# Performance work log

Hardware: AMD Instinct MI355X
Metric: run time of the kernel (lower is better)

## Reference

```python
import jax, jax.numpy as jnp
import numpy as np

MAG = 1.0
TAU = 0.5
B, D, C = 8192, 256, 128


def setup_inputs() -> dict:
    key = jax.random.key(0)
    k1, k2 = jax.random.split(key)
    outputs = jax.random.normal(k1, (B, D), dtype=jnp.float32)
    labels = jax.random.normal(k2, (B, C), dtype=jnp.float32)
    return {"outputs": outputs, "labels": labels}


def reference(outputs, labels):
    # Cosine-similarity matrix of labels, min-max normalized to [0, 1]
    norm2labels = labels / (jnp.linalg.norm(labels, axis=1, keepdims=True) + 1e-12)
    sim_mat = norm2labels @ norm2labels.T  # [B, B]
    sim_mat = (sim_mat - sim_mat.min()) / (sim_mat.max() - sim_mat.min())

    # Pairwise Euclidean distances of outputs via the Gram trick
    # ||x_i - x_j||^2 = ||x_i||^2 + ||x_j||^2 - 2 <x_i, x_j>
    sq = jnp.sum(outputs * outputs, axis=1)  # [B]
    d2 = sq[:, None] + sq[None, :] - 2.0 * (outputs @ outputs.T)  # [B, B]
    d2 = jnp.maximum(d2, 0.0)
    nz = d2 > 0.0
    # safe sqrt: zero (diagonal) entries get distance 0 with zero gradient,
    # matching torch.norm's subgradient at 0
    eud = jnp.sqrt(jnp.where(nz, d2, 1.0)) * nz
    eud = eud / eud.max()

    distance = eud + sim_mat  # [B, B]
    pos_mask = sim_mat > TAU

    # Per-row masked log-sum-exp terms (distance in [0, 2], no overflow risk)
    pos_loss = jnp.log(jnp.sum(jnp.where(pos_mask, jnp.exp(distance), 0.0), axis=1))
    neg_loss = jnp.log(jnp.sum(jnp.where(pos_mask, 0.0, jnp.exp(MAG - distance)), axis=1))

    # clamp negatives (and -inf from empty masks) to 0, as the original `if < 0` does
    loss = jnp.maximum(pos_loss, 0.0) + jnp.maximum(neg_loss, 0.0)
    return jnp.mean(loss)
```

## Files before the change

### kernel.cpp

```cpp
#include <hip/hip_runtime.h>
#include <hip/hip_bf16.h>


#define B_N 8192
#define NT   64
#define TILE 128
#define NTRI 2080
#define WS_NEEDED 142704704ull

typedef __attribute__((ext_vector_type(8))) short bf16x8;
typedef __attribute__((ext_vector_type(4))) float f32x4;
typedef __attribute__((ext_vector_type(2))) _Float16 f16x2;
typedef __attribute__((ext_vector_type(4))) unsigned u32x4;

typedef const __attribute__((address_space(1))) void g_void;
typedef __attribute__((address_space(3))) void l_void;

__device__ __forceinline__ unsigned fenc(float f) {
    unsigned u = __float_as_uint(f);
    return (u & 0x80000000u) ? ~u : (u | 0x80000000u);
}
__device__ __forceinline__ float fdec(unsigned k) {
    unsigned u = (k & 0x80000000u) ? (k ^ 0x80000000u) : ~k;
    return __uint_as_float(u);
}
__device__ __forceinline__ unsigned pack2(float a, float b) {
    f16x2 p; p[0] = (_Float16)a; p[1] = (_Float16)b;
    return *(unsigned*)&p;
}

__device__ __forceinline__ void tile_decode(int b, int& bi, int& bj) {
    int si, sj, ti, tj;
    if (b < 544) {
        int sb = b / 136, w = b - sb * 136;
        int i = 0;
        while (w >= 16 - i) { w -= 16 - i; i++; }
        si = sb; sj = sb; ti = i; tj = i + w;
    } else {
        int q = (b - 544) >> 8, w = (b - 544) & 255;
        int i = 0;
        while (q >= 3 - i) { q -= 3 - i; i++; }
        si = i; sj = i + 1 + q;
        ti = w >> 4; tj = w & 15;
    }
    bi = si * 16 + ti; bj = sj * 16 + tj;
}

__global__ __launch_bounds__(256) void prep_kernel(
    const float* __restrict__ outputs, const float* __restrict__ labels,
    __hip_bfloat16* __restrict__ Obp, __hip_bfloat16* __restrict__ Lnp,
    float* __restrict__ sq, float* __restrict__ pos_sums,
    float* __restrict__ neg_sums, unsigned* __restrict__ stats) {
    int g = blockIdx.x, tid = threadIdx.x;
    int rl = tid >> 4, c = tid & 15;
    int row = g * 16 + rl;
    __shared__ __align__(16) short tO[16][264];
    __shared__ __align__(16) short tL[16][136];

    float s = 0.f;
    #pragma unroll
    for (int k = 0; k < 4; k++) {
        f32x4 v = *(const f32x4*)&outputs[(size_t)row * 256 + c * 16 + k * 4];
        s += v[0]*v[0] + v[1]*v[1] + v[2]*v[2] + v[3]*v[3];
        __hip_bfloat16 b4[4];
        #pragma unroll
        for (int i = 0; i < 4; i++) b4[i] = __float2bfloat16(v[i]);
        *(uint2*)&tO[rl][c * 16 + k * 4] = *(uint2*)b4;
    }
    #pragma unroll
    for (int m = 1; m < 16; m <<= 1) s += __shfl_xor(s, m);
    if (c == 0) sq[row] = s;

    float ls = 0.f;
    f32x4 u0 = *(const f32x4*)&labels[(size_t)row * 128 + c * 8];
    f32x4 u1 = *(const f32x4*)&labels[(size_t)row * 128 + c * 8 + 4];
    ls += u0[0]*u0[0] + u0[1]*u0[1] + u0[2]*u0[2] + u0[3]*u0[3];
    ls += u1[0]*u1[0] + u1[1]*u1[1] + u1[2]*u1[2] + u1[3]*u1[3];
    #pragma unroll
    for (int m = 1; m < 16; m <<= 1) ls += __shfl_xor(ls, m);
    float inv = 1.f / (sqrtf(ls) + 1e-12f);
    {
        __hip_bfloat16 b4[4];
        #pragma unroll
        for (int i = 0; i < 4; i++) b4[i] = __float2bfloat16(u0[i] * inv);
        *(uint2*)&tL[rl][c * 8] = *(uint2*)b4;
        #pragma unroll
        for (int i = 0; i < 4; i++) b4[i] = __float2bfloat16(u1[i] * inv);
        *(uint2*)&tL[rl][c * 8 + 4] = *(uint2*)b4;
    }
    if (tid < 16) { pos_sums[g * 16 + tid] = 0.f; neg_sums[g * 16 + tid] = 0.f; }
    if (g == 0 && tid == 0) {
        stats[0] = 0xFFFFFFFFu; stats[1] = 0u; stats[2] = 0u;
    }
    __syncthreads();

    #pragma unroll
    for (int q = 0; q < 2; q++) {
        int sl = tid * 2 + q;
        int o = sl >> 4, rr = sl & 15;
        uint4 d = *(uint4*)&tO[rr][o * 8];
        *(uint4*)&Obp[(size_t)g * 4096 + (size_t)sl * 8] = d;
    }
    {
        int o = tid >> 4, rr = tid & 15;
        uint4 d = *(uint4*)&tL[rr][o * 8];
        *(uint4*)&Lnp[(size_t)g * 2048 + (size_t)tid * 8] = d;
    }
}

template<int KD8>
__device__ __forceinline__ void stage_slice(
    const short* __restrict__ P, int g0, int o0, short* L, int tid) {
    #pragma unroll
    for (int p = 0; p < 4; p++) {
        int u = p * 256 + tid;
        int gl = u >> 7, off = u & 127;
        size_t gu = ((size_t)(g0 + gl) * KD8 + o0) * 16 + off;
        __builtin_amdgcn_global_load_lds((g_void*)(P + gu * 8),
                                         (l_void*)(L + (size_t)u * 8), 16, 0, 0);
    }
}

__device__ __forceinline__ void mfma_slice(
    const short* As, const short* Bs, int wm4, int wn4,
    int l15, int quad, f32x4 (&acc)[4][4]) {
    #pragma unroll
    for (int kc = 0; kc < 2; kc++) {
        bf16x8 a[4], b[4];
        #pragma unroll
        for (int mi = 0; mi < 4; mi++)
            a[mi] = *(const bf16x8*)&As[((wm4 + mi) * 128
                                         + (kc * 4 + quad) * 16 + l15) * 8];
        #pragma unroll
        for (int ni = 0; ni < 4; ni++)
            b[ni] = *(const bf16x8*)&Bs[((wn4 + ni) * 128
                                         + (kc * 4 + quad) * 16 + l15) * 8];
        #pragma unroll
        for (int mi = 0; mi < 4; mi++)
            #pragma unroll
            for (int ni = 0; ni < 4; ni++)
                acc[mi][ni] = __builtin_amdgcn_mfma_f32_16x16x32_bf16(
                    a[mi], b[ni], acc[mi][ni], 0, 0, 0);
    }
}

__device__ __forceinline__ void zero_acc(f32x4 (&acc)[4][4]) {
    #pragma unroll
    for (int mi = 0; mi < 4; mi++)
        #pragma unroll
        for (int ni = 0; ni < 4; ni++) {
            f32x4 z = {0.f, 0.f, 0.f, 0.f};
            acc[mi][ni] = z;
        }
}

template<int KD8, int NS>
__device__ __forceinline__ void gram_staged(
    const short* __restrict__ P, int gA0, int gB0,
    short* As, short* Bs, int tid, int wm4, int wn4,
    int l15, int quad, f32x4 (&acc)[4][4]) {
    #pragma unroll
    for (int s = 0; s < NS; s++) {
        __syncthreads();
        stage_slice<KD8>(P, gA0, s * 8, As, tid);
        stage_slice<KD8>(P, gB0, s * 8, Bs, tid);
        __syncthreads();
        mfma_slice(As, Bs, wm4, wn4, l15, quad, acc);
    }
}

__global__ __launch_bounds__(256, 2) void stats_kernel(
    const short* __restrict__ Lnp, const short* __restrict__ Obp,
    const float* __restrict__ sq, unsigned* __restrict__ stats,
    unsigned* __restrict__ simT, unsigned* __restrict__ eudT, int store) {
    int bi, bj;
    tile_decode(blockIdx.x, bi, bj);
    int tid = threadIdx.x, lane = tid & 63, wid = tid >> 6;
    int wm = (wid >> 1) * 64, wn = (wid & 1) * 64;
    int wm4 = (wid >> 1) * 4, wn4 = (wid & 1) * 4;
    int l15 = lane & 15, quad = lane >> 4;
    int rB = bi * TILE, cB = bj * TILE;
    size_t tB = (size_t)blockIdx.x * 8192 + (size_t)tid * 4;

    __shared__ __align__(16) short As[1024 * 8];
    __shared__ __align__(16) short Bs[1024 * 8];

    float lmin = 1e30f, lmax = -1e30f, dmax = 0.f;
    f32x4 acc[4][4];

    zero_acc(acc);
    gram_staged<16, 2>(Lnp, bi * 8, bj * 8, As, Bs, tid, wm4, wn4, l15, quad, acc);
    #pragma unroll
    for (int mi = 0; mi < 4; mi++) {
        u32x4 v0, v1;
        #pragma unroll
        for (int ni = 0; ni < 4; ni++)
            #pragma unroll
            for (int h = 0; h < 2; h++) {
                float s0 = acc[mi][ni][2 * h], s1 = acc[mi][ni][2 * h + 1];
                lmin = fminf(lmin, fminf(s0, s1));
                lmax = fmaxf(lmax, fmaxf(s0, s1));
                int j = ni * 2 + h;
                unsigned pk = pack2(s0, s1);
                if (j < 4) v0[j] = pk; else v1[j - 4] = pk;
            }
        if (store) {
            __builtin_nontemporal_store(v0, (u32x4*)(simT + tB + (mi * 2 + 0) * 1024));
            __builtin_nontemporal_store(v1, (u32x4*)(simT + tB + (mi * 2 + 1) * 1024));
        }
    }

    zero_acc(acc);
    gram_staged<32, 4>(Obp, bi * 8, bj * 8, As, Bs, tid, wm4, wn4, l15, quad, acc);
    float sqj[4];
    #pragma unroll
    for (int ni = 0; ni < 4; ni++) sqj[ni] = sq[cB + wn + ni * 16 + l15];
    #pragma unroll
    for (int mi = 0; mi < 4; mi++) {
        f32x4 sqi = *(const f32x4*)&sq[rB + wm + mi * 16 + quad * 4];
        u32x4 v0, v1;
        #pragma unroll
        for (int ni = 0; ni < 4; ni++)
            #pragma unroll
            for (int h = 0; h < 2; h++) {
                float d20 = fmaxf(sqi[2*h]   + sqj[ni] - 2.f * acc[mi][ni][2*h],   0.f);
                float d21 = fmaxf(sqi[2*h+1] + sqj[ni] - 2.f * acc[mi][ni][2*h+1], 0.f);
                dmax = fmaxf(dmax, fmaxf(d20, d21));
                float e0 = (d20 > 0.f) ? sqrtf(d20) : 0.f;
                float e1 = (d21 > 0.f) ? sqrtf(d21) : 0.f;
                int j = ni * 2 + h;
                unsigned pk = pack2(e0, e1);
                if (j < 4) v0[j] = pk; else v1[j - 4] = pk;
            }
        if (store) {
            __builtin_nontemporal_store(v0, (u32x4*)(eudT + tB + (mi * 2 + 0) * 1024));
            __builtin_nontemporal_store(v1, (u32x4*)(eudT + tB + (mi * 2 + 1) * 1024));
        }
    }

    #pragma unroll
    for (int m = 1; m < 64; m <<= 1) {
        lmin = fminf(lmin, __shfl_xor(lmin, m));
        lmax = fmaxf(lmax, __shfl_xor(lmax, m));
        dmax = fmaxf(dmax, __shfl_xor(dmax, m));
    }
    __shared__ float red[3][4];
    if ((tid & 63) == 0) { red[0][wid] = lmin; red[1][wid] = lmax; red[2][wid] = dmax; }
    __syncthreads();
    if (tid == 0) {
        lmin = fminf(fminf(red[0][0], red[0][1]), fminf(red[0][2], red[0][3]));
        lmax = fmaxf(fmaxf(red[1][0], red[1][1]), fmaxf(red[1][2], red[1][3]));
        dmax = fmaxf(fmaxf(red[2][0], red[2][1]), fmaxf(red[2][2], red[2][3]));
        atomicMin(&stats[0], fenc(lmin));
        atomicMax(&stats[1], fenc(lmax));
        atomicMax(&stats[2], fenc(dmax));
    }
}

__global__ __launch_bounds__(256) void loss_stream_kernel(
    const unsigned* __restrict__ simT, const unsigned* __restrict__ eudT,
    const unsigned* __restrict__ stats,
    float* __restrict__ pos_sums, float* __restrict__ neg_sums) {
    int bi, bj;
    tile_decode(blockIdx.x, bi, bj);
    int tid = threadIdx.x, lane = tid & 63, wid = tid >> 6;
    int wm = (wid >> 1) * 64, wn = (wid & 1) * 64;
    int l15 = lane & 15, quad = lane >> 4;
    size_t tB = (size_t)blockIdx.x * 8192 + (size_t)tid * 4;

    float smin = fdec(stats[0]);
    float smax = fdec(stats[1]);
    float d2max = fdec(stats[2]);
    float invr = 1.f / (smax - smin);
    float invem = rsqrtf(d2max);

    __shared__ float rP[TILE][2], rN[TILE][2];
    __shared__ float cP[TILE][2], cN[TILE][2];
    float cpsum[4] = {0.f, 0.f, 0.f, 0.f};
    float cnsum[4] = {0.f, 0.f, 0.f, 0.f};

    #pragma unroll
    for (int mi = 0; mi < 4; mi++) {
        u32x4 s0 = __builtin_nontemporal_load((const u32x4*)(simT + tB + (mi * 2 + 0) * 1024));
        u32x4 s1 = __builtin_nontemporal_load((const u32x4*)(simT + tB + (mi * 2 + 1) * 1024));
        u32x4 e0 = __builtin_nontemporal_load((const u32x4*)(eudT + tB + (mi * 2 + 0) * 1024));
        u32x4 e1 = __builtin_nontemporal_load((const u32x4*)(eudT + tB + (mi * 2 + 1) * 1024));
        float ps[4] = {0.f, 0.f, 0.f, 0.f};
        float ns[4] = {0.f, 0.f, 0.f, 0.f};
        #pragma unroll
        for (int j = 0; j < 8; j++) {
            unsigned sv = (j < 4) ? s0[j] : s1[j - 4];
            unsigned ev = (j < 4) ? e0[j] : e1[j - 4];
            int ni = j >> 1, h = j & 1;
            f16x2 spair = *(f16x2*)&sv;
            f16x2 epair = *(f16x2*)&ev;
            #pragma unroll
            for (int e = 0; e < 2; e++) {
                float sn = ((float)spair[e] - smin) * invr;
                float dist = (float)epair[e] * invem + sn;
                bool pos = sn > 0.5f;
                float pv = pos ? __expf(dist) : 0.f;
                float nv = pos ? 0.f : __expf(1.0f - dist);
                ps[2 * h + e] += pv;  ns[2 * h + e] += nv;
                cpsum[ni] += pv;  cnsum[ni] += nv;
            }
        }
        #pragma unroll
        for (int r = 0; r < 4; r++) {
            #pragma unroll
            for (int m = 1; m < 16; m <<= 1) {
                ps[r] += __shfl_xor(ps[r], m);
                ns[r] += __shfl_xor(ns[r], m);
            }
            if (l15 == 0) {
                int rr = wm + mi * 16 + quad * 4 + r;
                rP[rr][wid & 1] = ps[r];
                rN[rr][wid & 1] = ns[r];
            }
        }
    }
    #pragma unroll
    for (int ni = 0; ni < 4; ni++) {
        #pragma unroll
        for (int m = 16; m < 64; m <<= 1) {
            cpsum[ni] += __shfl_xor(cpsum[ni], m);
            cnsum[ni] += __shfl_xor(cnsum[ni], m);
        }
        if (quad == 0) {
            int cc = wn + ni * 16 + l15;
            cP[cc][wid >> 1] = cpsum[ni];
            cN[cc][wid >> 1] = cnsum[ni];
        }
    }
    __syncthreads();
    if (tid < TILE) {
        atomicAdd(&pos_sums[bi * TILE + tid], rP[tid][0] + rP[tid][1]);
        atomicAdd(&neg_sums[bi * TILE + tid], rN[tid][0] + rN[tid][1]);
        if (bi != bj) {
            atomicAdd(&pos_sums[bj * TILE + tid], cP[tid][0] + cP[tid][1]);
            atomicAdd(&neg_sums[bj * TILE + tid], cN[tid][0] + cN[tid][1]);
        }
    }
}

__global__ __launch_bounds__(256, 2) void loss_recompute_kernel(
    const short* __restrict__ Lnp, const short* __restrict__ Obp,
    const float* __restrict__ sq, const unsigned* __restrict__ stats,
    float* __restrict__ pos_sums, float* __restrict__ neg_sums) {
    int bi, bj;
    tile_decode(blockIdx.x, bi, bj);
    int tid = threadIdx.x, lane = tid & 63, wid = tid >> 6;
    int wm = (wid >> 1) * 64, wn = (wid & 1) * 64;
    int wm4 = (wid >> 1) * 4, wn4 = (wid & 1) * 4;
    int l15 = lane & 15, quad = lane >> 4;
    int rB = bi * TILE, cB = bj * TILE;

    __shared__ __align__(16) short As[1024 * 8];
    __shared__ __align__(16) short Bs[1024 * 8];
    __shared__ unsigned simW[256 * 33];
    __shared__ float rP[TILE][2], rN[TILE][2];
    __shared__ float cP[TILE][2], cN[TILE][2];
    unsigned* my = &simW[tid * 33];

    f32x4 acc[4][4];

    zero_acc(acc);
    gram_staged<16, 2>(Lnp, bi * 8, bj * 8, As, Bs, tid, wm4, wn4, l15, quad, acc);
    #pragma unroll
    for (int mi = 0; mi < 4; mi++)
        #pragma unroll
        for (int ni = 0; ni < 4; ni++) {
            my[(mi * 4 + ni) * 2 + 0] = pack2(acc[mi][ni][0], acc[mi][ni][1]);
            my[(mi * 4 + ni) * 2 + 1] = pack2(acc[mi][ni][2], acc[mi][ni][3]);
        }

    zero_acc(acc);
    gram_staged<32, 4>(Obp, bi * 8, bj * 8, As, Bs, tid, wm4, wn4, l15, quad, acc);

    float smin = fdec(stats[0]);
    float smax = fdec(stats[1]);
    float d2max = fdec(stats[2]);
    float invr = 1.f / (smax - smin);
    float invem = rsqrtf(d2max);

    float sqj[4];
    #pragma unroll
    for (int ni = 0; ni < 4; ni++) sqj[ni] = sq[cB + wn + ni * 16 + l15];
    float cpsum[4] = {0.f, 0.f, 0.f, 0.f};
    float cnsum[4] = {0.f, 0.f, 0.f, 0.f};

    #pragma unroll
    for (int mi = 0; mi < 4; mi++) {
        f32x4 sqi = *(const f32x4*)&sq[rB + wm + mi * 16 + quad * 4];
        float ps[4] = {0.f, 0.f, 0.f, 0.f};
        float ns[4] = {0.f, 0.f, 0.f, 0.f};
        #pragma unroll
        for (int ni = 0; ni < 4; ni++) {
            f16x2 s01 = ((const f16x2*)my)[(mi * 4 + ni) * 2 + 0];
            f16x2 s23 = ((const f16x2*)my)[(mi * 4 + ni) * 2 + 1];
            #pragma unroll
            for (int r = 0; r < 4; r++) {
                float sraw = (r < 2) ? (float)s01[r] : (float)s23[r - 2];
                float sn = (sraw - smin) * invr;
                float g = acc[mi][ni][r];
                float d2 = fmaxf(sqi[r] + sqj[ni] - 2.f * g, 0.f);
                float eud = (d2 > 0.f) ? sqrtf(d2) * invem : 0.f;
                float dist = eud + sn;
                bool pos = sn > 0.5f;
                float pv = pos ? __expf(dist) : 0.f;
                float nv = pos ? 0.f : __expf(1.0f - dist);
                ps[r] += pv;  ns[r] += nv;
                cpsum[ni] += pv;  cnsum[ni] += nv;
            }
        }
        #pragma unroll
        for (int r = 0; r < 4; r++) {
            #pragma unroll
            for (int m = 1; m < 16; m <<= 1) {
                ps[r] += __shfl_xor(ps[r], m);
                ns[r] += __shfl_xor(ns[r], m);
            }
            if (l15 == 0) {
                int rr = wm + mi * 16 + quad * 4 + r;
                rP[rr][wid & 1] = ps[r];
                rN[rr][wid & 1] = ns[r];
            }
        }
    }
    #pragma unroll
    for (int ni = 0; ni < 4; ni++) {
        #pragma unroll
        for (int m = 16; m < 64; m <<= 1) {
            cpsum[ni] += __shfl_xor(cpsum[ni], m);
            cnsum[ni] += __shfl_xor(cnsum[ni], m);
        }
        if (quad == 0) {
            int cc = wn + ni * 16 + l15;
            cP[cc][wid >> 1] = cpsum[ni];
            cN[cc][wid >> 1] = cnsum[ni];
        }
    }
    __syncthreads();
    if (tid < TILE) {
        atomicAdd(&pos_sums[bi * TILE + tid], rP[tid][0] + rP[tid][1]);
        atomicAdd(&neg_sums[bi * TILE + tid], rN[tid][0] + rN[tid][1]);
        if (bi != bj) {
            atomicAdd(&pos_sums[bj * TILE + tid], cP[tid][0] + cP[tid][1]);
            atomicAdd(&neg_sums[bj * TILE + tid], cN[tid][0] + cN[tid][1]);
        }
    }
}

__global__ __launch_bounds__(256) void finalize_kernel(
    const float* __restrict__ pos_sums, const float* __restrict__ neg_sums,
    float* __restrict__ out) {
    int t = threadIdx.x;
    float acc = 0.f;
    for (int i = t; i < B_N; i += 256) {
        float p = pos_sums[i], n = neg_sums[i];
        float pl = fmaxf(logf(p), 0.f);
        float nl = (n > 0.f) ? fmaxf(logf(n), 0.f) : 0.f;
        acc += pl + nl;
    }
    #pragma unroll
    for (int m = 1; m < 64; m <<= 1) acc += __shfl_xor(acc, m);
    __shared__ float w4[4];
    if ((t & 63) == 0) w4[t >> 6] = acc;
    __syncthreads();
    if (t == 0) out[0] = (w4[0] + w4[1] + w4[2] + w4[3]) / (float)B_N;
}

extern "C" void kernel_launch(void* const* d_in, const int* in_sizes, int n_in,
                              void* d_out, int out_size, void* d_ws, size_t ws_size,
                              hipStream_t stream) {
    const float* outputs = (const float*)d_in[0];
    const float* labels  = (const float*)d_in[1];
    float* out = (float*)d_out;
    char* ws = (char*)d_ws;
    __hip_bfloat16* Obp = (__hip_bfloat16*)(ws);
    __hip_bfloat16* Lnp = (__hip_bfloat16*)(ws + 4194304);
    float* sq           = (float*)(ws + 6291456);
    float* pos_sums     = (float*)(ws + 6324224);
    float* neg_sums     = (float*)(ws + 6356992);
    unsigned* stats     = (unsigned*)(ws + 6389760);
    unsigned* simT      = (unsigned*)(ws + 6389824);
    unsigned* eudT      = (unsigned*)(ws + 74547264);
    int big = (ws_size >= WS_NEEDED) ? 1 : 0;

    prep_kernel<<<B_N / 16, 256, 0, stream>>>(outputs, labels, Obp, Lnp, sq,
                                              pos_sums, neg_sums, stats);
    stats_kernel<<<NTRI, 256, 0, stream>>>((const short*)Lnp, (const short*)Obp,
                                           sq, stats, simT, eudT, big);
    if (big)
        loss_stream_kernel<<<NTRI, 256, 0, stream>>>(simT, eudT, stats,
                                                     pos_sums, neg_sums);
    else
        loss_recompute_kernel<<<NTRI, 256, 0, stream>>>((const short*)Lnp,
                                                        (const short*)Obp,
                                                        sq, stats,
                                                        pos_sums, neg_sums);
    finalize_kernel<<<1, 256, 0, stream>>>(pos_sums, neg_sums, out);
}
```

Baseline: 209.6 us.

## Compute stats with 256x256 super-tiles and double-buffered LDS staging

The stats kernel now processes 256x256 super-tiles with 512 threads (8 waves, 128x64 per wave), launching 528 upper-triangular blocks instead of 2080 128x128 tiles. Each block stages K-slices into double-buffered LDS via global_load_lds and overlaps the next slice's loads with MFMA on the current one. Results are still written in the original 128-tile layout through a tile_encode mapping, and the redundant lower-triangle sub-tile on diagonal super-tiles is skipped. Larger tiles give more operand reuse and fewer blocks. In exchange, each wave holds many more accumulator registers and each block uses 128 KB of LDS, which limits occupancy, and the diagonal super-tiles compute one sub-tile that is thrown away.

```diff
diff --git a/kernel.cpp b/kernel.cpp
--- a/kernel.cpp
+++ b/kernel.cpp
@@ -3,9 +3,9 @@
 
 
 #define B_N 8192
-#define NT   64
 #define TILE 128
 #define NTRI 2080
+#define NSUP 528
 #define WS_NEEDED 142704704ull
 
 typedef __attribute__((ext_vector_type(8))) short bf16x8;
@@ -46,6 +46,13 @@
     bi = si * 16 + ti; bj = sj * 16 + tj;
 }
 
+__device__ __forceinline__ int tile_encode(int bi, int bj) {
+    int si = bi >> 4, sj = bj >> 4, ti = bi & 15, tj = bj & 15;
+    if (si == sj) return si * 136 + ti * 16 - (ti * (ti - 1)) / 2 + (tj - ti);
+    int off = 3 * si - (si * (si - 1)) / 2 + (sj - si - 1);
+    return 544 + off * 256 + ti * 16 + tj;
+}
+
 __global__ __launch_bounds__(256) void prep_kernel(
     const float* __restrict__ outputs, const float* __restrict__ labels,
     __hip_bfloat16* __restrict__ Obp, __hip_bfloat16* __restrict__ Lnp,
@@ -169,72 +176,167 @@
     }
 }
 
-__global__ __launch_bounds__(256, 2) void stats_kernel(
+__device__ __forceinline__ void stage512(const short* __restrict__ P, int g0,
+                                         int kd8, int o0, short* L, int tid) {
+    #pragma unroll
+    for (int p = 0; p < 4; p++) {
+        int u = p * 512 + tid;
+        int gl = u >> 7, off = u & 127;
+        size_t gu = ((size_t)(g0 + gl) * kd8 + o0) * 16 + off;
+        __builtin_amdgcn_global_load_lds((g_void*)(P + gu * 8),
+                                         (l_void*)(L + (size_t)u * 8), 16, 0, 0);
+    }
+}
+
+__device__ __forceinline__ void mfma64(const short* As, const short* Bs,
+                                       int wr8, int wc4, int l15, int quad,
+                                       f32x4 (&acc)[8][4]) {
+    #pragma unroll
+    for (int kc = 0; kc < 2; kc++) {
+        bf16x8 a[8], b[4];
+        #pragma unroll
+        for (int am = 0; am < 8; am++)
+            a[am] = *(const bf16x8*)&As[((wr8 + am) * 128
+                                         + (kc * 4 + quad) * 16 + l15) * 8];
+        #pragma unroll
+        for (int bn = 0; bn < 4; bn++)
+            b[bn] = *(const bf16x8*)&Bs[((wc4 + bn) * 128
+                                         + (kc * 4 + quad) * 16 + l15) * 8];
+        #pragma unroll
+        for (int am = 0; am < 8; am++)
+            #pragma unroll
+            for (int bn = 0; bn < 4; bn++)
+                acc[am][bn] = __builtin_amdgcn_mfma_f32_16x16x32_bf16(
+                    a[am], b[bn], acc[am][bn], 0, 0, 0);
+    }
+}
+
+__device__ __forceinline__ void zero_acc8(f32x4 (&acc)[8][4]) {
+    #pragma unroll
+    for (int mi = 0; mi < 8; mi++)
+        #pragma unroll
+        for (int ni = 0; ni < 4; ni++) {
+            f32x4 z = {0.f, 0.f, 0.f, 0.f};
+            acc[mi][ni] = z;
+        }
+}
+
+#define VMCNT(n) asm volatile("s_waitcnt vmcnt(" #n ")" ::: "memory")
+#define BAR() __builtin_amdgcn_s_barrier()
+
+__global__ __launch_bounds__(512, 2) void stats_kernel(
     const short* __restrict__ Lnp, const short* __restrict__ Obp,
     const float* __restrict__ sq, unsigned* __restrict__ stats,
     unsigned* __restrict__ simT, unsigned* __restrict__ eudT, int store) {
-    int bi, bj;
-    tile_decode(blockIdx.x, bi, bj);
+    int bt = blockIdx.x, BI = 0;
+    while (bt >= 32 - BI) { bt -= 32 - BI; BI++; }
+    int BJ = BI + bt;
+
     int tid = threadIdx.x, lane = tid & 63, wid = tid >> 6;
-    int wm = (wid >> 1) * 64, wn = (wid & 1) * 64;
-    int wm4 = (wid >> 1) * 4, wn4 = (wid & 1) * 4;
+    int wr = wid >> 2, wc = wid & 3;
     int l15 = lane & 15, quad = lane >> 4;
-    int rB = bi * TILE, cB = bj * TILE;
-    size_t tB = (size_t)blockIdx.x * 8192 + (size_t)tid * 4;
-
-    __shared__ __align__(16) short As[1024 * 8];
-    __shared__ __align__(16) short Bs[1024 * 8];
+    int wr8 = wr * 8, wc4 = wc * 4;
+    int wcH = wc >> 1, wcL = wc & 1;
+
+    __shared__ __align__(16) short As[2][16384];
+    __shared__ __align__(16) short Bs[2][16384];
+    __shared__ float red[3][8];
+
+    int gA = BI * 16, gB = BJ * 16;
+    bool dostore = store && !(BI == BJ && wr == 1 && wcH == 0);
+    int b128 = tile_encode(BI * 2 + wr, BJ * 2 + wcH);
+    size_t blkbase = (size_t)b128 * 8192;
 
     float lmin = 1e30f, lmax = -1e30f, dmax = 0.f;
-    f32x4 acc[4][4];
-
-    zero_acc(acc);
-    gram_staged<16, 2>(Lnp, bi * 8, bj * 8, As, Bs, tid, wm4, wn4, l15, quad, acc);
-    #pragma unroll
-    for (int mi = 0; mi < 4; mi++) {
-        u32x4 v0, v1;
-        #pragma unroll
-        for (int ni = 0; ni < 4; ni++)
-            #pragma unroll
-            for (int h = 0; h < 2; h++) {
-                float s0 = acc[mi][ni][2 * h], s1 = acc[mi][ni][2 * h + 1];
-                lmin = fminf(lmin, fminf(s0, s1));
-                lmax = fmaxf(lmax, fmaxf(s0, s1));
-                int j = ni * 2 + h;
-                unsigned pk = pack2(s0, s1);
-                if (j < 4) v0[j] = pk; else v1[j - 4] = pk;
-            }
-        if (store) {
-            __builtin_nontemporal_store(v0, (u32x4*)(simT + tB + (mi * 2 + 0) * 1024));
-            __builtin_nontemporal_store(v1, (u32x4*)(simT + tB + (mi * 2 + 1) * 1024));
-        }
-    }
-
-    zero_acc(acc);
-    gram_staged<32, 4>(Obp, bi * 8, bj * 8, As, Bs, tid, wm4, wn4, l15, quad, acc);
-    float sqj[4];
-    #pragma unroll
-    for (int ni = 0; ni < 4; ni++) sqj[ni] = sq[cB + wn + ni * 16 + l15];
-    #pragma unroll
-    for (int mi = 0; mi < 4; mi++) {
-        f32x4 sqi = *(const f32x4*)&sq[rB + wm + mi * 16 + quad * 4];
-        u32x4 v0, v1;
-        #pragma unroll
-        for (int ni = 0; ni < 4; ni++)
-            #pragma unroll
-            for (int h = 0; h < 2; h++) {
-                float d20 = fmaxf(sqi[2*h]   + sqj[ni] - 2.f * acc[mi][ni][2*h],   0.f);
-                float d21 = fmaxf(sqi[2*h+1] + sqj[ni] - 2.f * acc[mi][ni][2*h+1], 0.f);
-                dmax = fmaxf(dmax, fmaxf(d20, d21));
-                float e0 = (d20 > 0.f) ? sqrtf(d20) : 0.f;
-                float e1 = (d21 > 0.f) ? sqrtf(d21) : 0.f;
-                int j = ni * 2 + h;
-                unsigned pk = pack2(e0, e1);
-                if (j < 4) v0[j] = pk; else v1[j - 4] = pk;
-            }
-        if (store) {
-            __builtin_nontemporal_store(v0, (u32x4*)(eudT + tB + (mi * 2 + 0) * 1024));
-            __builtin_nontemporal_store(v1, (u32x4*)(eudT + tB + (mi * 2 + 1) * 1024));
+    f32x4 acc[8][4];
+
+    zero_acc8(acc);
+    stage512(Lnp, gA, 16, 0, &As[0][0], tid);
+    stage512(Lnp, gB, 16, 0, &Bs[0][0], tid);
+    stage512(Lnp, gA, 16, 8, &As[1][0], tid);
+    stage512(Lnp, gB, 16, 8, &Bs[1][0], tid);
+    VMCNT(8); BAR();
+    mfma64(&As[0][0], &Bs[0][0], wr8, wc4, l15, quad, acc);
+    VMCNT(0); BAR();
+    mfma64(&As[1][0], &Bs[1][0], wr8, wc4, l15, quad, acc);
+
+    #pragma unroll
+    for (int am = 0; am < 8; am++) {
+        int tid128 = (((am >> 2) << 1) | wcL) * 64 + lane;
+        #pragma unroll
+        for (int bh = 0; bh < 2; bh++) {
+            u32x4 v;
+            #pragma unroll
+            for (int b2 = 0; b2 < 2; b2++) {
+                int bn = bh * 2 + b2;
+                #pragma unroll
+                for (int h = 0; h < 2; h++) {
+                    float s0 = acc[am][bn][2 * h], s1 = acc[am][bn][2 * h + 1];
+                    lmin = fminf(lmin, fminf(s0, s1));
+                    lmax = fmaxf(lmax, fmaxf(s0, s1));
+                    v[b2 * 2 + h] = pack2(s0, s1);
+                }
+            }
+            if (dostore)
+                __builtin_nontemporal_store(v, (u32x4*)(simT + blkbase
+                    + ((am & 3) * 2 + bh) * 1024 + tid128 * 4));
+        }
+    }
+    BAR();
+
+    zero_acc8(acc);
+    stage512(Obp, gA, 32, 0, &As[0][0], tid);
+    stage512(Obp, gB, 32, 0, &Bs[0][0], tid);
+    stage512(Obp, gA, 32, 8, &As[1][0], tid);
+    stage512(Obp, gB, 32, 8, &Bs[1][0], tid);
+    VMCNT(8); BAR();
+    mfma64(&As[0][0], &Bs[0][0], wr8, wc4, l15, quad, acc);
+    VMCNT(0); BAR();
+    stage512(Obp, gA, 32, 16, &As[0][0], tid);
+    stage512(Obp, gB, 32, 16, &Bs[0][0], tid);
+    mfma64(&As[1][0], &Bs[1][0], wr8, wc4, l15, quad, acc);
+    VMCNT(0); BAR();
+    stage512(Obp, gA, 32, 24, &As[1][0], tid);
+    stage512(Obp, gB, 32, 24, &Bs[1][0], tid);
+    f32x4 sqi[8]; float sqj[4];
+    {
+        int rqa = BI * 256 + wr * 128 + quad * 4;
+        int cqa = BJ * 256 + wc * 64 + l15;
+        #pragma unroll
+        for (int am = 0; am < 8; am++)
+            sqi[am] = *(const f32x4*)&sq[rqa + am * 16];
+        #pragma unroll
+        for (int bn = 0; bn < 4; bn++)
+            sqj[bn] = sq[cqa + bn * 16];
+    }
+    mfma64(&As[0][0], &Bs[0][0], wr8, wc4, l15, quad, acc);
+    VMCNT(0); BAR();
+    mfma64(&As[1][0], &Bs[1][0], wr8, wc4, l15, quad, acc);
+
+    #pragma unroll
+    for (int am = 0; am < 8; am++) {
+        int tid128 = (((am >> 2) << 1) | wcL) * 64 + lane;
+        f32x4 si = sqi[am];
+        #pragma unroll
+        for (int bh = 0; bh < 2; bh++) {
+            u32x4 v;
+            #pragma unroll
+            for (int b2 = 0; b2 < 2; b2++) {
+                int bn = bh * 2 + b2;
+                float sj = sqj[bn];
+                #pragma unroll
+                for (int h = 0; h < 2; h++) {
+                    float d20 = fmaxf(si[2*h]   + sj - 2.f * acc[am][bn][2*h],   0.f);
+                    float d21 = fmaxf(si[2*h+1] + sj - 2.f * acc[am][bn][2*h+1], 0.f);
+                    dmax = fmaxf(dmax, fmaxf(d20, d21));
+                    float e0 = (d20 > 0.f) ? sqrtf(d20) : 0.f;
+                    float e1 = (d21 > 0.f) ? sqrtf(d21) : 0.f;
+                    v[b2 * 2 + h] = pack2(e0, e1);
+                }
+            }
+            if (dostore)
+                __builtin_nontemporal_store(v, (u32x4*)(eudT + blkbase
+                    + ((am & 3) * 2 + bh) * 1024 + tid128 * 4));
         }
     }
 
@@ -244,13 +346,16 @@
         lmax = fmaxf(lmax, __shfl_xor(lmax, m));
         dmax = fmaxf(dmax, __shfl_xor(dmax, m));
     }
-    __shared__ float red[3][4];
-    if ((tid & 63) == 0) { red[0][wid] = lmin; red[1][wid] = lmax; red[2][wid] = dmax; }
+    if (lane == 0) { red[0][wid] = lmin; red[1][wid] = lmax; red[2][wid] = dmax; }
     __syncthreads();
     if (tid == 0) {
-        lmin = fminf(fminf(red[0][0], red[0][1]), fminf(red[0][2], red[0][3]));
-        lmax = fmaxf(fmaxf(red[1][0], red[1][1]), fmaxf(red[1][2], red[1][3]));
-        dmax = fmaxf(fmaxf(red[2][0], red[2][1]), fmaxf(red[2][2], red[2][3]));
+        lmin = red[0][0]; lmax = red[1][0]; dmax = red[2][0];
+        #pragma unroll
+        for (int w = 1; w < 8; w++) {
+            lmin = fminf(lmin, red[0][w]);
+            lmax = fmaxf(lmax, red[1][w]);
+            dmax = fmaxf(dmax, red[2][w]);
+        }
         atomicMin(&stats[0], fenc(lmin));
         atomicMax(&stats[1], fenc(lmax));
         atomicMax(&stats[2], fenc(dmax));
@@ -489,7 +594,7 @@
 
     prep_kernel<<<B_N / 16, 256, 0, stream>>>(outputs, labels, Obp, Lnp, sq,
                                               pos_sums, neg_sums, stats);
-    stats_kernel<<<NTRI, 256, 0, stream>>>((const short*)Lnp, (const short*)Obp,
+    stats_kernel<<<NSUP, 512, 0, stream>>>((const short*)Lnp, (const short*)Obp,
                                            sq, stats, simT, eudT, big);
     if (big)
         loss_stream_kernel<<<NTRI, 256, 0, stream>>>(simT, eudT, stats,
```

After: 268.8 us. 28.2% more time.

## Double-buffer LDS staging in stats kernel and overlap loads with MFMA and epilogue

Applied to the files above, without the earlier changes.

Replaces the synchronous stage-then-compute loops in the stats kernel with a hand-scheduled double-buffered pipeline. Global-to-LDS slice loads for the next step, including the first output-Gram slices, are issued before the current MFMA slice and before the label epilogue, using explicit vmcnt waits and raw barriers. The aim is to hide global load latency behind MFMA and epilogue work. The cost is doubled LDS use (64KB per block), which may limit the two-blocks-per-CU occupancy, plus fragile hand-counted vmcnt values.

```diff
diff --git a/kernel.cpp b/kernel.cpp
--- a/kernel.cpp
+++ b/kernel.cpp
@@ -3,7 +3,6 @@
 
 
 #define B_N 8192
-#define NT   64
 #define TILE 128
 #define NTRI 2080
 #define WS_NEEDED 142704704ull
@@ -169,6 +168,10 @@
     }
 }
 
+#define VMCNT(n) asm volatile("s_waitcnt vmcnt(" #n ")" ::: "memory")
+#define BAR() __builtin_amdgcn_s_barrier()
+#define FENCE() asm volatile("" ::: "memory")
+
 __global__ __launch_bounds__(256, 2) void stats_kernel(
     const short* __restrict__ Lnp, const short* __restrict__ Obp,
     const float* __restrict__ sq, unsigned* __restrict__ stats,
@@ -182,14 +185,30 @@
     int rB = bi * TILE, cB = bj * TILE;
     size_t tB = (size_t)blockIdx.x * 8192 + (size_t)tid * 4;
 
-    __shared__ __align__(16) short As[1024 * 8];
-    __shared__ __align__(16) short Bs[1024 * 8];
+    __shared__ __align__(16) short As[2][8192];
+    __shared__ __align__(16) short Bs[2][8192];
+    __shared__ float red[3][4];
 
     float lmin = 1e30f, lmax = -1e30f, dmax = 0.f;
     f32x4 acc[4][4];
 
     zero_acc(acc);
-    gram_staged<16, 2>(Lnp, bi * 8, bj * 8, As, Bs, tid, wm4, wn4, l15, quad, acc);
+    stage_slice<16>(Lnp, bi * 8, 0, As[0], tid);
+    stage_slice<16>(Lnp, bj * 8, 0, Bs[0], tid);
+    stage_slice<16>(Lnp, bi * 8, 8, As[1], tid);
+    stage_slice<16>(Lnp, bj * 8, 8, Bs[1], tid);
+    VMCNT(8); BAR();
+    mfma_slice(As[0], Bs[0], wm4, wn4, l15, quad, acc);
+    BAR();
+    stage_slice<32>(Obp, bi * 8, 0, As[0], tid);
+    stage_slice<32>(Obp, bj * 8, 0, Bs[0], tid);
+    VMCNT(8); BAR();
+    mfma_slice(As[1], Bs[1], wm4, wn4, l15, quad, acc);
+    BAR();
+    stage_slice<32>(Obp, bi * 8, 8, As[1], tid);
+    stage_slice<32>(Obp, bj * 8, 8, Bs[1], tid);
+    FENCE();
+
     #pragma unroll
     for (int mi = 0; mi < 4; mi++) {
         u32x4 v0, v1;
@@ -211,13 +230,31 @@
     }
 
     zero_acc(acc);
-    gram_staged<32, 4>(Obp, bi * 8, bj * 8, As, Bs, tid, wm4, wn4, l15, quad, acc);
-    float sqj[4];
+    VMCNT(24); BAR();
+    mfma_slice(As[0], Bs[0], wm4, wn4, l15, quad, acc);
+    BAR();
+    stage_slice<32>(Obp, bi * 8, 16, As[0], tid);
+    stage_slice<32>(Obp, bj * 8, 16, Bs[0], tid);
+    FENCE();
+    float sqj[4]; f32x4 sqi4[4];
     #pragma unroll
     for (int ni = 0; ni < 4; ni++) sqj[ni] = sq[cB + wn + ni * 16 + l15];
     #pragma unroll
+    for (int mi = 0; mi < 4; mi++)
+        sqi4[mi] = *(const f32x4*)&sq[rB + wm + mi * 16 + quad * 4];
+    VMCNT(32); BAR();
+    mfma_slice(As[1], Bs[1], wm4, wn4, l15, quad, acc);
+    BAR();
+    stage_slice<32>(Obp, bi * 8, 24, As[1], tid);
+    stage_slice<32>(Obp, bj * 8, 24, Bs[1], tid);
+    VMCNT(8); BAR();
+    mfma_slice(As[0], Bs[0], wm4, wn4, l15, quad, acc);
+    VMCNT(0); BAR();
+    mfma_slice(As[1], Bs[1], wm4, wn4, l15, quad, acc);
+
+    #pragma unroll
     for (int mi = 0; mi < 4; mi++) {
-        f32x4 sqi = *(const f32x4*)&sq[rB + wm + mi * 16 + quad * 4];
+        f32x4 sqi = sqi4[mi];
         u32x4 v0, v1;
         #pragma unroll
         for (int ni = 0; ni < 4; ni++)
@@ -244,7 +281,6 @@
         lmax = fmaxf(lmax, __shfl_xor(lmax, m));
         dmax = fmaxf(dmax, __shfl_xor(dmax, m));
     }
-    __shared__ float red[3][4];
     if ((tid & 63) == 0) { red[0][wid] = lmin; red[1][wid] = lmax; red[2][wid] = dmax; }
     __syncthreads();
     if (tid == 0) {
```

Result: no change. 209.6 us (-0.0%).

## Rework stats kernel into 256x256 super-tiles with double-buffered async LDS staging

Applied to the files above, without the earlier changes.

The stats kernel now launches 528 blocks of 1024 threads, each covering a 256x256 upper-triangular super-tile made of four 128x128 sub-tiles, instead of 2080 blocks of 256 threads. Operand slices are loaded with global_load_lds into double-buffered shared memory under manual vmcnt waits, so the label and output Gram loads overlap MFMA work. Each staged A/B panel is reused across two sub-tiles. Stores are remapped through tile_encode so the existing loss kernel layout still holds, and the redundant lower sub-tile on diagonal blocks is skipped. The cost is a very large shared-memory footprint per block, lower occupancy, and fragile hand-counted vmcnt values.

```diff
diff --git a/kernel.cpp b/kernel.cpp
--- a/kernel.cpp
+++ b/kernel.cpp
@@ -3,9 +3,9 @@
 
 
 #define B_N 8192
-#define NT   64
 #define TILE 128
 #define NTRI 2080
+#define NSUP 528
 #define WS_NEEDED 142704704ull
 
 typedef __attribute__((ext_vector_type(8))) short bf16x8;
@@ -46,6 +46,13 @@
     bi = si * 16 + ti; bj = sj * 16 + tj;
 }
 
+__device__ __forceinline__ int tile_encode(int bi, int bj) {
+    int si = bi >> 4, sj = bj >> 4, ti = bi & 15, tj = bj & 15;
+    if (si == sj) return si * 136 + ti * 16 - (ti * (ti - 1)) / 2 + (tj - ti);
+    int off = 3 * si - (si * (si - 1)) / 2 + (sj - si - 1);
+    return 544 + off * 256 + ti * 16 + tj;
+}
+
 __global__ __launch_bounds__(256) void prep_kernel(
     const float* __restrict__ outputs, const float* __restrict__ labels,
     __hip_bfloat16* __restrict__ Obp, __hip_bfloat16* __restrict__ Lnp,
@@ -169,27 +176,67 @@
     }
 }
 
-__global__ __launch_bounds__(256, 2) void stats_kernel(
+__device__ __forceinline__ void stage1024(const short* __restrict__ P, int g0,
+                                          int kd8, int o0, short* L, int tid) {
+    #pragma unroll
+    for (int p = 0; p < 2; p++) {
+        int u = p * 1024 + tid;
+        int gl = u >> 7, off = u & 127;
+        size_t gu = ((size_t)(g0 + gl) * kd8 + o0) * 16 + off;
+        __builtin_amdgcn_global_load_lds((g_void*)(P + gu * 8),
+                                         (l_void*)(L + (size_t)u * 8), 16, 0, 0);
+    }
+}
+
+#define VMCNT(n) asm volatile("s_waitcnt vmcnt(" #n ")" ::: "memory")
+#define BAR() __builtin_amdgcn_s_barrier()
+#define FENCE() asm volatile("" ::: "memory")
+
+__global__ __launch_bounds__(1024, 4) void stats_kernel(
     const short* __restrict__ Lnp, const short* __restrict__ Obp,
     const float* __restrict__ sq, unsigned* __restrict__ stats,
     unsigned* __restrict__ simT, unsigned* __restrict__ eudT, int store) {
-    int bi, bj;
-    tile_decode(blockIdx.x, bi, bj);
+    int bt = blockIdx.x, BI = 0;
+    while (bt >= 32 - BI) { bt -= 32 - BI; BI++; }
+    int BJ = BI + bt;
+
     int tid = threadIdx.x, lane = tid & 63, wid = tid >> 6;
-    int wm = (wid >> 1) * 64, wn = (wid & 1) * 64;
-    int wm4 = (wid >> 1) * 4, wn4 = (wid & 1) * 4;
+    int wr = wid >> 2, wc = wid & 3;
+    int tr = wr >> 1, tc = wc >> 1;
     int l15 = lane & 15, quad = lane >> 4;
-    int rB = bi * TILE, cB = bj * TILE;
-    size_t tB = (size_t)blockIdx.x * 8192 + (size_t)tid * 4;
-
-    __shared__ __align__(16) short As[1024 * 8];
-    __shared__ __align__(16) short Bs[1024 * 8];
+    int wm4 = wr * 4, wn4 = wc * 4;
+
+    __shared__ __align__(16) short As[2][16384];
+    __shared__ __align__(16) short Bs[2][16384];
+    __shared__ float red[3][16];
+
+    int gA = BI * 16, gB = BJ * 16;
+    bool dostore = store && !(BI == BJ && tr == 1 && tc == 0);
+    int b128 = tile_encode(BI * 2 + tr, BJ * 2 + tc);
+    int wid0 = ((wr & 1) << 1) | (wc & 1);
+    int tid128 = wid0 * 64 + lane;
+    size_t blkbase = (size_t)b128 * 8192 + (size_t)tid128 * 4;
 
     float lmin = 1e30f, lmax = -1e30f, dmax = 0.f;
     f32x4 acc[4][4];
 
     zero_acc(acc);
-    gram_staged<16, 2>(Lnp, bi * 8, bj * 8, As, Bs, tid, wm4, wn4, l15, quad, acc);
+    stage1024(Lnp, gA, 16, 0, &As[0][0], tid);
+    stage1024(Lnp, gB, 16, 0, &Bs[0][0], tid);
+    stage1024(Lnp, gA, 16, 8, &As[1][0], tid);
+    stage1024(Lnp, gB, 16, 8, &Bs[1][0], tid);
+    VMCNT(4); BAR();
+    mfma_slice(&As[0][0], &Bs[0][0], wm4, wn4, l15, quad, acc);
+    BAR();
+    stage1024(Obp, gA, 32, 0, &As[0][0], tid);
+    stage1024(Obp, gB, 32, 0, &Bs[0][0], tid);
+    VMCNT(4); BAR();
+    mfma_slice(&As[1][0], &Bs[1][0], wm4, wn4, l15, quad, acc);
+    BAR();
+    stage1024(Obp, gA, 32, 8, &As[1][0], tid);
+    stage1024(Obp, gB, 32, 8, &Bs[1][0], tid);
+    FENCE();
+
     #pragma unroll
     for (int mi = 0; mi < 4; mi++) {
         u32x4 v0, v1;
@@ -204,20 +251,47 @@
                 unsigned pk = pack2(s0, s1);
                 if (j < 4) v0[j] = pk; else v1[j - 4] = pk;
             }
-        if (store) {
-            __builtin_nontemporal_store(v0, (u32x4*)(simT + tB + (mi * 2 + 0) * 1024));
-            __builtin_nontemporal_store(v1, (u32x4*)(simT + tB + (mi * 2 + 1) * 1024));
-        }
-    }
+        if (dostore) {
+            __builtin_nontemporal_store(v0, (u32x4*)(simT + blkbase + (mi * 2 + 0) * 1024));
+            __builtin_nontemporal_store(v1, (u32x4*)(simT + blkbase + (mi * 2 + 1) * 1024));
+        }
+    }
+    FENCE();
 
     zero_acc(acc);
-    gram_staged<32, 4>(Obp, bi * 8, bj * 8, As, Bs, tid, wm4, wn4, l15, quad, acc);
-    float sqj[4];
-    #pragma unroll
-    for (int ni = 0; ni < 4; ni++) sqj[ni] = sq[cB + wn + ni * 16 + l15];
+    if (dostore) { VMCNT(12); } else { VMCNT(4); }
+    BAR();
+    mfma_slice(&As[0][0], &Bs[0][0], wm4, wn4, l15, quad, acc);
+    BAR();
+    stage1024(Obp, gA, 32, 16, &As[0][0], tid);
+    stage1024(Obp, gB, 32, 16, &Bs[0][0], tid);
+    FENCE();
+    float sqj[4]; f32x4 sqi4[4];
+    {
+        int rqa = BI * 256 + wr * 64 + quad * 4;
+        int cqa = BJ * 256 + wc * 64 + l15;
+        #pragma unroll
+        for (int mi = 0; mi < 4; mi++)
+            sqi4[mi] = *(const f32x4*)&sq[rqa + mi * 16];
+        #pragma unroll
+        for (int ni = 0; ni < 4; ni++)
+            sqj[ni] = sq[cqa + ni * 16];
+    }
+    FENCE();
+    if (dostore) { VMCNT(20); } else { VMCNT(12); }
+    BAR();
+    mfma_slice(&As[1][0], &Bs[1][0], wm4, wn4, l15, quad, acc);
+    BAR();
+    stage1024(Obp, gA, 32, 24, &As[1][0], tid);
+    stage1024(Obp, gB, 32, 24, &Bs[1][0], tid);
+    VMCNT(12); BAR();
+    mfma_slice(&As[0][0], &Bs[0][0], wm4, wn4, l15, quad, acc);
+    VMCNT(0); BAR();
+    mfma_slice(&As[1][0], &Bs[1][0], wm4, wn4, l15, quad, acc);
+
     #pragma unroll
     for (int mi = 0; mi < 4; mi++) {
-        f32x4 sqi = *(const f32x4*)&sq[rB + wm + mi * 16 + quad * 4];
+        f32x4 sqi = sqi4[mi];
         u32x4 v0, v1;
         #pragma unroll
         for (int ni = 0; ni < 4; ni++)
@@ -232,9 +306,9 @@
                 unsigned pk = pack2(e0, e1);
                 if (j < 4) v0[j] = pk; else v1[j - 4] = pk;
             }
-        if (store) {
-            __builtin_nontemporal_store(v0, (u32x4*)(eudT + tB + (mi * 2 + 0) * 1024));
-            __builtin_nontemporal_store(v1, (u32x4*)(eudT + tB + (mi * 2 + 1) * 1024));
+        if (dostore) {
+            __builtin_nontemporal_store(v0, (u32x4*)(eudT + blkbase + (mi * 2 + 0) * 1024));
+            __builtin_nontemporal_store(v1, (u32x4*)(eudT + blkbase + (mi * 2 + 1) * 1024));
         }
     }
 
@@ -244,13 +318,16 @@
         lmax = fmaxf(lmax, __shfl_xor(lmax, m));
         dmax = fmaxf(dmax, __shfl_xor(dmax, m));
     }
-    __shared__ float red[3][4];
-    if ((tid & 63) == 0) { red[0][wid] = lmin; red[1][wid] = lmax; red[2][wid] = dmax; }
+    if (lane == 0) { red[0][wid] = lmin; red[1][wid] = lmax; red[2][wid] = dmax; }
     __syncthreads();
     if (tid == 0) {
-        lmin = fminf(fminf(red[0][0], red[0][1]), fminf(red[0][2], red[0][3]));
-        lmax = fmaxf(fmaxf(red[1][0], red[1][1]), fmaxf(red[1][2], red[1][3]));
-        dmax = fmaxf(fmaxf(red[2][0], red[2][1]), fmaxf(red[2][2], red[2][3]));
+        lmin = red[0][0]; lmax = red[1][0]; dmax = red[2][0];
+        #pragma unroll
+        for (int w = 1; w < 16; w++) {
+            lmin = fminf(lmin, red[0][w]);
+            lmax = fmaxf(lmax, red[1][w]);
+            dmax = fmaxf(dmax, red[2][w]);
+        }
         atomicMin(&stats[0], fenc(lmin));
         atomicMax(&stats[1], fenc(lmax));
         atomicMax(&stats[2], fenc(dmax));
@@ -489,8 +566,8 @@
 
     prep_kernel<<<B_N / 16, 256, 0, stream>>>(outputs, labels, Obp, Lnp, sq,
                                               pos_sums, neg_sums, stats);
-    stats_kernel<<<NTRI, 256, 0, stream>>>((const short*)Lnp, (const short*)Obp,
-                                           sq, stats, simT, eudT, big);
+    stats_kernel<<<NSUP, 1024, 0, stream>>>((const short*)Lnp, (const short*)Obp,
+                                            sq, stats, simT, eudT, big);
     if (big)
         loss_stream_kernel<<<NTRI, 256, 0, stream>>>(simT, eudT, stats,
                                                      pos_sums, neg_sums);
```

After: 268.0 us. +27.9%, slower.
